# Performance work log

Hardware: AMD Instinct MI355X
Metric: run time of the kernel (lower is better)

The kernel has to match this reference:

```python
import jax, jax.numpy as jnp
import numpy as np

N_USERS = 8192
D = 128
E = 262144        # known edges (nonzero_idx rows)
K = 131072        # static pad size for data-dependent candidate extraction
COS_THR = 0.3
TAU = 0.2


def setup_inputs() -> dict:
    key = jax.random.key(0)
    k1, k2, k3, k4 = jax.random.split(key, 4)
    user_emb = jax.random.normal(k1, (N_USERS, D), dtype=jnp.float32)
    nonzero_idx = jax.random.randint(k2, (E, 2), 0, N_USERS)
    W = jax.random.normal(k3, (2, 2 * D), dtype=jnp.float32) * 0.05  # mlp_s weight [2, 2*latent]
    b = jnp.zeros((2,), dtype=jnp.float32)                            # mlp_s bias
    gumbel_noise = jax.random.gumbel(k4, (E + K, 2), dtype=jnp.float32)
    return {"user_emb": user_emb, "W": W, "b": b,
            "gumbel_noise": gumbel_noise, "nonzero_idx": nonzero_idx}


def reference(user_emb, W, b, gumbel_noise, nonzero_idx):
    n = user_emb.shape[0]
    # ---- get_candidate_pair ----
    norm = jnp.linalg.norm(user_emb, axis=1, keepdims=True)
    u = user_emb / jnp.maximum(norm, 1e-12)          # F.normalize(dim=1)
    cos = u @ u.T                                    # [n, n]
    diag = jnp.arange(n)
    cos = cos.at[diag, diag].set(-1.0)               # fill_diagonal_(-1)
    cos = cos.at[nonzero_idx[:, 0], nonzero_idx[:, 1]].set(-1.0)
    mask = cos > COS_THR
    # static-size nonzero; padded slots point at (0,0) where cos == -1,
    # so they behave as invalid candidates (weight 0 downstream).
    ci, cj = jnp.nonzero(mask, size=K, fill_value=0)
    cand_vals = cos[ci, cj]                          # padded entries = -1
    cand_idx = jnp.stack([ci, cj], axis=1)           # [K, 2]

    # ---- forward ----
    pair_idx = jnp.concatenate([nonzero_idx, cand_idx], axis=0)   # [E+K, 2]
    u_emb = user_emb[pair_idx[:, 0]]
    v_emb = user_emb[pair_idx[:, 1]]
    concat_emb = jnp.concatenate([u_emb, v_emb], axis=1)          # [E+K, 2D]
    logits = concat_emb @ W.T + b                                 # [E+K, 2]

    # hard gumbel-softmax (straight-through)
    y_soft = jax.nn.softmax((logits + gumbel_noise) / TAU, axis=-1)
    y_hard = jax.nn.one_hot(jnp.argmax(y_soft, axis=-1), 2, dtype=y_soft.dtype)
    gumbel_output = y_hard + y_soft - jax.lax.stop_gradient(y_soft)
    gumbel_retain = gumbel_output[:, 0]                           # [E+K]

    # ---- get_edge_weight ----
    cand_w = jnp.maximum(cand_vals, 0.0)                          # masked_fill(<0, 0)
    weights = jnp.concatenate([jnp.ones((E,), dtype=cand_w.dtype), cand_w])
    w = gumbel_retain * weights                                   # [E+K]
    gumbel_01 = w
    gumbel_retain_w = jnp.concatenate([w[:, None], w[:, None]], axis=0)  # [2(E+K), 1]
    return gumbel_01, gumbel_retain_w, pair_idx
```

## Files before the change

### kernel.cpp

```cpp
#include <hip/hip_runtime.h>
#include <hip/hip_bf16.h>
#include <math.h>

#define N_USERS 8192
#define DIMS    128
#define EDGES   262144
#define KCAND   131072
#define NTOT    (EDGES + KCAND)
#define LISTCAP 131072
#define CAPB    2048
#define NTILES  528
#define COS_THR 0.3f
#define EPS_SEL 6e-3f
#define LOGIT_MARGIN 2e-3f
#define DEADKEY 0xFFFFFFFFu

typedef short bf16x8 __attribute__((ext_vector_type(8)));
typedef float f32x4  __attribute__((ext_vector_type(4)));


__global__ __launch_bounds__(256) void prep_k(const float* __restrict__ x,
                                              const float* __restrict__ W,
                                              const int* __restrict__ nz,
                                              float* __restrict__ un,
                                              unsigned short* __restrict__ u0,
                                              float4* __restrict__ P,
                                              unsigned* __restrict__ excl) {
  if (blockIdx.x < 256) {
#pragma clang fp contract(off)
    const int tid  = threadIdx.x;
    const int rloc = tid >> 3;
    const int j    = tid & 7;
    const int i    = blockIdx.x * 32 + rloc;
    const float* r = x + (size_t)i * DIMS;

    float vals[16];
    float a = 0.f;
#pragma unroll
    for (int b8 = 0; b8 < 16; ++b8) {
      float t = r[b8 * 8 + j];
      vals[b8] = t;
      a = a + t * t;
    }
    a = a + __shfl_xor(a, 1, 64);
    a = a + __shfl_xor(a, 2, 64);
    float s = a + __shfl_xor(a, 4, 64);
    float n = (float)sqrt((double)s);
    n = fmaxf(n, 1e-12f);

    unsigned short* slab = u0 + (size_t)(i >> 7) * 16384 + (i & 127) * 8;
    float p0 = 0.f, p1 = 0.f, p2 = 0.f, p3 = 0.f;
#pragma unroll
    for (int b8 = 0; b8 < 16; ++b8) {
      int k = b8 * 8 + j;
      float t = vals[b8];
      float v = t / n;
      un[(size_t)i * DIMS + k] = v;
      __hip_bfloat16 h = __float2bfloat16(v);
      slab[(size_t)b8 * 1024 + j] = *(unsigned short*)&h;
      p0 = fmaf(t, W[k], p0);
      p1 = fmaf(t, W[128 + k], p1);
      p2 = fmaf(t, W[256 + k], p2);
      p3 = fmaf(t, W[384 + k], p3);
    }
#pragma unroll
    for (int m = 1; m < 8; m <<= 1) {
      p0 += __shfl_xor(p0, m, 64);
      p1 += __shfl_xor(p1, m, 64);
      p2 += __shfl_xor(p2, m, 64);
      p3 += __shfl_xor(p3, m, 64);
    }
    if (j == 0) P[i] = make_float4(p0, p1, p2, p3);
  } else {
    int t = (blockIdx.x - 256) * 256 + threadIdx.x;
    if (t < EDGES) {
      uint2 e = ((const uint2*)nz)[t];
      atomicOr(&excl[(size_t)e.x * 256 + (e.y >> 5)], 1u << (e.y & 31));
    }
  }
}

__global__ __launch_bounds__(1024) void mfma_pass(const unsigned short* __restrict__ u0,
                                                  uint2* __restrict__ list,
                                                  int* __restrict__ gcount) {
  __shared__ __align__(16) unsigned short As[2][16][128][8];
  __shared__ __align__(16) unsigned short Bs[2][16][128][8];
  __shared__ uint2 svec[CAPB];
  __shared__ int lcnt, lbase;

  const int tid  = threadIdx.x;
  const int lane = tid & 63;
  const int wv   = tid >> 6;
  const int quad = lane >> 4;
  const int l15  = lane & 15;
  const int wm   = wv >> 2;
  const int wn   = wv & 3;

  int rem = blockIdx.x, cj = 0;
  while (rem >= cj + 1) { rem -= cj + 1; ++cj; }
  const int ri = rem;
  const int I0 = ri * 256, J0 = cj * 256;

  if (tid == 0) lcnt = 0;

  const uint4* __restrict__ Asrc = (const uint4*)(u0 + (size_t)ri * 32768);
  const uint4* __restrict__ Bsrc = (const uint4*)(u0 + (size_t)cj * 32768);
  uint4* Ad = (uint4*)As;
  uint4* Bd = (uint4*)Bs;
  {
    uint4 pA[4], pB[4];
#pragma unroll
    for (int it = 0; it < 4; ++it) {
      pA[it] = Asrc[it * 1024 + tid];
      pB[it] = Bsrc[it * 1024 + tid];
    }
#pragma unroll
    for (int it = 0; it < 4; ++it) {
      Ad[it * 1024 + tid] = pA[it];
      Bd[it * 1024 + tid] = pB[it];
    }
  }
  __syncthreads();

  f32x4 acc[4][4];
#pragma unroll
  for (int mt = 0; mt < 4; ++mt)
#pragma unroll
    for (int nt = 0; nt < 4; ++nt)
#pragma unroll
      for (int g = 0; g < 4; ++g) acc[mt][nt][g] = 0.f;

  const int aslab = wm >> 1, arow0 = (wm & 1) * 64;
  const int bslab = wn >> 1, brow0 = (wn & 1) * 64;

#pragma unroll
  for (int kc = 0; kc < 4; ++kc) {
    const int cq = kc * 4 + quad;
    bf16x8 af[4], bf[4];
#pragma unroll
    for (int mt = 0; mt < 4; ++mt)
      af[mt] = *(const bf16x8*)&As[aslab][cq][arow0 + mt * 16 + l15][0];
#pragma unroll
    for (int nt = 0; nt < 4; ++nt)
      bf[nt] = *(const bf16x8*)&Bs[bslab][cq][brow0 + nt * 16 + l15][0];
#pragma unroll
    for (int mt = 0; mt < 4; ++mt)
#pragma unroll
      for (int nt = 0; nt < 4; ++nt)
        acc[mt][nt] = __builtin_amdgcn_mfma_f32_16x16x32_bf16(
            af[mt], bf[nt], acc[mt][nt], 0, 0, 0);
  }

#pragma unroll
  for (int mt = 0; mt < 4; ++mt)
#pragma unroll
    for (int nt = 0; nt < 4; ++nt)
#pragma unroll
      for (int g = 0; g < 4; ++g) {
        float v = acc[mt][nt][g];
        if (v > COS_THR - EPS_SEL) {
          int i = I0 + wm * 64 + mt * 16 + quad * 4 + g;
          int j = J0 + wn * 64 + nt * 16 + l15;
          if (j > i) {
            int idx = atomicAdd(&lcnt, 2);
            if (idx + 1 < CAPB) {
              svec[idx]     = make_uint2(((unsigned)i << 13) | j,
                                         __float_as_uint(v));
              svec[idx + 1] = make_uint2(((unsigned)j << 13) | i,
                                         __float_as_uint(v));
            }
          }
        }
      }

  __syncthreads();
  int n = min(lcnt, CAPB);
  if (tid == 0) lbase = atomicAdd(gcount, n);
  __syncthreads();
  int base = lbase;
  for (int t = tid; t < n; t += 1024) {
    int o = base + t;
    if (o < LISTCAP) list[o] = svec[t];
  }
}

__global__ __launch_bounds__(256) void resolve_hist_k(const float* __restrict__ un,
                                                      const unsigned* __restrict__ excl,
                                                      uint2* __restrict__ list,
                                                      const int* __restrict__ gcount,
                                                      int* __restrict__ row_cnt) {
  int t = blockIdx.x * 256 + threadIdx.x;
  int n = min(*gcount, LISTCAP);
  if (t >= n) return;
  uint2 e = list[t];
  int i = e.x >> 13, j = e.x & 8191;
  unsigned word = excl[(size_t)i * 256 + (j >> 5)];
  bool alive = !((word >> (j & 31)) & 1u);
  float v = __uint_as_float(e.y);
  if (alive && v <= COS_THR + EPS_SEL) {
    const float* a = un + (size_t)i * DIMS;
    const float* b = un + (size_t)j * DIMS;
    float s = 0.f;
    for (int k = 0; k < DIMS; ++k) s = fmaf(a[k], b[k], s);
    alive = (s > COS_THR);
    if (alive) list[t] = make_uint2(e.x, __float_as_uint(s));
  }
  if (!alive) list[t] = make_uint2(DEADKEY, 0u);
  else        atomicAdd(&row_cnt[i], 1);
}

__global__ __launch_bounds__(256) void scan8k(const int* __restrict__ cnt,
                                              int* __restrict__ off) {
  __shared__ int sm[256];
  int t = threadIdx.x;
  int base = t * 32;
  int s = 0;
  for (int i = 0; i < 32; ++i) s += cnt[base + i];
  sm[t] = s;
  __syncthreads();
  int x = s;
  for (int d = 1; d < 256; d <<= 1) {
    int y = (t >= d) ? sm[t - d] : 0;
    __syncthreads();
    x += y;
    sm[t] = x;
    __syncthreads();
  }
  int run = x - s;
  for (int i = 0; i < 32; ++i) { off[base + i] = run; run += cnt[base + i]; }
  if (t == 255) off[N_USERS] = x;
}

__global__ __launch_bounds__(256) void scatter_k(const uint2* __restrict__ list,
                                                 const int* __restrict__ gcount,
                                                 const int* __restrict__ row_off,
                                                 int* __restrict__ row_pos,
                                                 int* __restrict__ cand_i,
                                                 int* __restrict__ cand_j,
                                                 float* __restrict__ cand_v) {
  int t = blockIdx.x * 256 + threadIdx.x;
  int n = min(*gcount, LISTCAP);
  if (t >= n) return;
  uint2 e = list[t];
  if (e.x == DEADKEY) return;
  int i = e.x >> 13, j = e.x & 8191;
  int pos = row_off[i] + atomicAdd(&row_pos[i], 1);
  if (pos < KCAND) {
    cand_i[pos] = i;
    cand_j[pos] = j;
    cand_v[pos] = __uint_as_float(e.y);
  }
}

__global__ __launch_bounds__(256) void sortrow_k(const int* __restrict__ row_off,
                                                 const int* __restrict__ row_cnt,
                                                 int* __restrict__ cand_j,
                                                 float* __restrict__ cand_v) {
  int r = blockIdx.x * 256 + threadIdx.x;
  if (r >= N_USERS) return;
  int o = row_off[r], c = row_cnt[r];
  if (o + c > KCAND) c = max(0, KCAND - o);
  for (int a = 1; a < c; ++a) {
    int jv = cand_j[o + a];
    float vv = cand_v[o + a];
    int b = a - 1;
    while (b >= 0 && cand_j[o + b] > jv) {
      cand_j[o + b + 1] = cand_j[o + b];
      cand_v[o + b + 1] = cand_v[o + b];
      --b;
    }
    cand_j[o + b + 1] = jv;
    cand_v[o + b + 1] = vv;
  }
}

__global__ __launch_bounds__(256) void finalize_k(const float* __restrict__ ue,
                                                  const float* __restrict__ W,
                                                  const float* __restrict__ b,
                                                  const float* __restrict__ g,
                                                  const int* __restrict__ nz,
                                                  const int* __restrict__ cand_i,
                                                  const int* __restrict__ cand_j,
                                                  const float* __restrict__ cand_v,
                                                  const int* __restrict__ row_off,
                                                  const float4* __restrict__ P,
                                                  float* __restrict__ out) {
  int p = blockIdx.x * 256 + threadIdx.x;
  if (p >= NTOT) return;

  int i, j;
  float wgt;
  if (p < EDGES) {
    i = nz[2 * p];
    j = nz[2 * p + 1];
    wgt = 1.0f;
  } else {
    int q = p - EDGES;
    if (q >= row_off[N_USERS]) {
      out[p] = 0.0f;
      out[NTOT + p] = 0.0f;
      out[2 * NTOT + p] = 0.0f;
      out[3 * NTOT + 2 * p + 0] = 0.0f;
      out[3 * NTOT + 2 * p + 1] = 0.0f;
      return;
    }
    i = cand_i[q];
    j = cand_j[q];
    wgt = fmaxf(cand_v[q], 0.0f);
  }

  float4 Pi = P[i], Pj = P[j];
  float l0 = Pi.x + Pj.y + b[0];
  float l1 = Pi.z + Pj.w + b[1];
  float g0 = g[2 * p], g1 = g[2 * p + 1];
  float s0 = l0 + g0, s1 = l1 + g1;

  if (fabsf(s0 - s1) < LOGIT_MARGIN) {
    const float* ri = ue + (size_t)i * DIMS;
    const float* rj = ue + (size_t)j * DIMS;
    float e0 = 0.f, e1 = 0.f;
    for (int k = 0; k < DIMS; ++k) {
      e0 = fmaf(ri[k], W[k], e0);
      e1 = fmaf(ri[k], W[256 + k], e1);
    }
    for (int k = 0; k < DIMS; ++k) {
      e0 = fmaf(rj[k], W[128 + k], e0);
      e1 = fmaf(rj[k], W[384 + k], e1);
    }
    s0 = (e0 + b[0]) + g0;
    s1 = (e1 + b[1]) + g1;
  }

  float w = (s0 >= s1) ? wgt : 0.0f;

  out[p] = w;
  out[NTOT + p] = w;
  out[2 * NTOT + p] = w;
  out[3 * NTOT + 2 * p + 0] = (float)i;
  out[3 * NTOT + 2 * p + 1] = (float)j;
}

extern "C" void kernel_launch(void* const* d_in, const int* in_sizes, int n_in,
                              void* d_out, int out_size, void* d_ws, size_t ws_size,
                              hipStream_t stream) {
  (void)in_sizes; (void)n_in; (void)out_size; (void)ws_size;

  const float* user_emb = (const float*)d_in[0];
  const float* W        = (const float*)d_in[1];
  const float* b        = (const float*)d_in[2];
  const float* gnoise   = (const float*)d_in[3];
  const int*   nz       = (const int*)d_in[4];
  float* out = (float*)d_out;

  char* ws = (char*)d_ws;
  float*          un      = (float*)(ws + 0);
  unsigned short* u0      = (unsigned short*)(ws + (4u << 20));
  unsigned*       excl    = (unsigned*)(ws + (6u << 20));
  char*           zbase   = ws + (14u << 20);
  int*            gcount  = (int*)(zbase);
  int*            row_cnt = (int*)(zbase + 64);
  int*            row_pos = (int*)(zbase + 64 + 32768);
  int*            row_off = (int*)(ws + (14u << 20) + (96u << 10));
  uint2*          list    = (uint2*)(ws + (15u << 20));
  int*            cand_i  = (int*)(ws + (16u << 20));
  int*            cand_j  = (int*)(ws + (16u << 20) + (512u << 10));
  float*          cand_v  = (float*)(ws + (17u << 20));
  float4*         P       = (float4*)(ws + (17u << 20) + (512u << 10));

  hipMemsetAsync(excl, 0, (8u << 20) + (96u << 10), stream);

  prep_k<<<256 + EDGES / 256, 256, 0, stream>>>(user_emb, W, nz, un, u0, P, excl);
  mfma_pass<<<NTILES, 1024, 0, stream>>>(u0, list, gcount);
  resolve_hist_k<<<LISTCAP / 256, 256, 0, stream>>>(un, excl, list, gcount,
                                                    row_cnt);
  scan8k<<<1, 256, 0, stream>>>(row_cnt, row_off);
  scatter_k<<<LISTCAP / 256, 256, 0, stream>>>(list, gcount, row_off, row_pos,
                                               cand_i, cand_j, cand_v);
  sortrow_k<<<N_USERS / 256, 256, 0, stream>>>(row_off, row_cnt, cand_j, cand_v);
  finalize_k<<<NTOT / 256, 256, 0, stream>>>(user_emb, W, b, gnoise, nz,
                                             cand_i, cand_j, cand_v, row_off,
                                             P, out);
}
```

Measured before the change: 139.2 us.

## Fuse scan, scatter, row sort and finalize into one tail kernel

```diff
diff --git a/kernel.cpp b/kernel.cpp
--- a/kernel.cpp
+++ b/kernel.cpp
@@ -209,106 +209,13 @@
   else        atomicAdd(&row_cnt[i], 1);
 }
 
-__global__ __launch_bounds__(256) void scan8k(const int* __restrict__ cnt,
-                                              int* __restrict__ off) {
-  __shared__ int sm[256];
-  int t = threadIdx.x;
-  int base = t * 32;
-  int s = 0;
-  for (int i = 0; i < 32; ++i) s += cnt[base + i];
-  sm[t] = s;
-  __syncthreads();
-  int x = s;
-  for (int d = 1; d < 256; d <<= 1) {
-    int y = (t >= d) ? sm[t - d] : 0;
-    __syncthreads();
-    x += y;
-    sm[t] = x;
-    __syncthreads();
-  }
-  int run = x - s;
-  for (int i = 0; i < 32; ++i) { off[base + i] = run; run += cnt[base + i]; }
-  if (t == 255) off[N_USERS] = x;
-}
-
-__global__ __launch_bounds__(256) void scatter_k(const uint2* __restrict__ list,
-                                                 const int* __restrict__ gcount,
-                                                 const int* __restrict__ row_off,
-                                                 int* __restrict__ row_pos,
-                                                 int* __restrict__ cand_i,
-                                                 int* __restrict__ cand_j,
-                                                 float* __restrict__ cand_v) {
-  int t = blockIdx.x * 256 + threadIdx.x;
-  int n = min(*gcount, LISTCAP);
-  if (t >= n) return;
-  uint2 e = list[t];
-  if (e.x == DEADKEY) return;
-  int i = e.x >> 13, j = e.x & 8191;
-  int pos = row_off[i] + atomicAdd(&row_pos[i], 1);
-  if (pos < KCAND) {
-    cand_i[pos] = i;
-    cand_j[pos] = j;
-    cand_v[pos] = __uint_as_float(e.y);
-  }
-}
-
-__global__ __launch_bounds__(256) void sortrow_k(const int* __restrict__ row_off,
-                                                 const int* __restrict__ row_cnt,
-                                                 int* __restrict__ cand_j,
-                                                 float* __restrict__ cand_v) {
-  int r = blockIdx.x * 256 + threadIdx.x;
-  if (r >= N_USERS) return;
-  int o = row_off[r], c = row_cnt[r];
-  if (o + c > KCAND) c = max(0, KCAND - o);
-  for (int a = 1; a < c; ++a) {
-    int jv = cand_j[o + a];
-    float vv = cand_v[o + a];
-    int b = a - 1;
-    while (b >= 0 && cand_j[o + b] > jv) {
-      cand_j[o + b + 1] = cand_j[o + b];
-      cand_v[o + b + 1] = cand_v[o + b];
-      --b;
-    }
-    cand_j[o + b + 1] = jv;
-    cand_v[o + b + 1] = vv;
-  }
-}
-
-__global__ __launch_bounds__(256) void finalize_k(const float* __restrict__ ue,
-                                                  const float* __restrict__ W,
-                                                  const float* __restrict__ b,
-                                                  const float* __restrict__ g,
-                                                  const int* __restrict__ nz,
-                                                  const int* __restrict__ cand_i,
-                                                  const int* __restrict__ cand_j,
-                                                  const float* __restrict__ cand_v,
-                                                  const int* __restrict__ row_off,
-                                                  const float4* __restrict__ P,
-                                                  float* __restrict__ out) {
-  int p = blockIdx.x * 256 + threadIdx.x;
-  if (p >= NTOT) return;
-
-  int i, j;
-  float wgt;
-  if (p < EDGES) {
-    i = nz[2 * p];
-    j = nz[2 * p + 1];
-    wgt = 1.0f;
-  } else {
-    int q = p - EDGES;
-    if (q >= row_off[N_USERS]) {
-      out[p] = 0.0f;
-      out[NTOT + p] = 0.0f;
-      out[2 * NTOT + p] = 0.0f;
-      out[3 * NTOT + 2 * p + 0] = 0.0f;
-      out[3 * NTOT + 2 * p + 1] = 0.0f;
-      return;
-    }
-    i = cand_i[q];
-    j = cand_j[q];
-    wgt = fmaxf(cand_v[q], 0.0f);
-  }
-
+__device__ __forceinline__ void emit_out(int p, int i, int j, float wgt,
+                                         const float4* __restrict__ P,
+                                         const float* __restrict__ b,
+                                         const float* __restrict__ g,
+                                         const float* __restrict__ ue,
+                                         const float* __restrict__ W,
+                                         float* __restrict__ out) {
   float4 Pi = P[i], Pj = P[j];
   float l0 = Pi.x + Pj.y + b[0];
   float l1 = Pi.z + Pj.w + b[1];
@@ -332,12 +239,122 @@
   }
 
   float w = (s0 >= s1) ? wgt : 0.0f;
-
   out[p] = w;
   out[NTOT + p] = w;
   out[2 * NTOT + p] = w;
   out[3 * NTOT + 2 * p + 0] = (float)i;
   out[3 * NTOT + 2 * p + 1] = (float)j;
+}
+
+__global__ __launch_bounds__(256) void tail_k(const uint2* __restrict__ list,
+                                              const int* __restrict__ gcount,
+                                              const int* __restrict__ row_cnt,
+                                              int* __restrict__ cand_i,
+                                              int* __restrict__ cand_j,
+                                              float* __restrict__ cand_v,
+                                              const float* __restrict__ ue,
+                                              const float* __restrict__ W,
+                                              const float* __restrict__ b,
+                                              const float* __restrict__ g,
+                                              const int* __restrict__ nz,
+                                              const float4* __restrict__ P,
+                                              float* __restrict__ out) {
+  __shared__ int s_chunk[256];
+  __shared__ int s_off[32];
+  __shared__ int s_pos[32];
+  __shared__ int s_lo, s_M;
+
+  const int tid = threadIdx.x;
+  const int bo  = blockIdx.x;
+
+  int s = 0;
+  {
+    const int rb = tid * 32;
+    for (int k = 0; k < 32; ++k) s += row_cnt[rb + k];
+  }
+  s_chunk[tid] = s;
+  __syncthreads();
+  int x = s;
+  for (int d = 1; d < 256; d <<= 1) {
+    int y = (tid >= d) ? s_chunk[tid - d] : 0;
+    __syncthreads();
+    x += y;
+    s_chunk[tid] = x;
+    __syncthreads();
+  }
+  if (tid == 255) s_M = x;
+  if (tid == bo)  s_lo = x - s;
+  __syncthreads();
+  if (tid == 0) {
+    int run = s_lo;
+    for (int k = 0; k < 32; ++k) {
+      s_off[k] = run;
+      run += row_cnt[bo * 32 + k];
+    }
+  }
+  if (tid < 32) s_pos[tid] = 0;
+  __syncthreads();
+
+  const int n = min(*gcount, LISTCAP);
+  const int M = s_M;
+
+  for (int t = tid; t < n; t += 256) {
+    uint2 e = list[t];
+    if (e.x == DEADKEY) continue;
+    int i = e.x >> 13;
+    if ((i >> 5) == bo) {
+      int lr = i & 31;
+      int pos = s_off[lr] + atomicAdd(&s_pos[lr], 1);
+      if (pos < KCAND) {
+        cand_i[pos] = i;
+        cand_j[pos] = e.x & 8191;
+        cand_v[pos] = __uint_as_float(e.y);
+      }
+    }
+  }
+  __syncthreads();
+
+  if (tid < 32) {
+    int o = s_off[tid], c = s_pos[tid];
+    if (o + c > KCAND) c = max(0, KCAND - o);
+    for (int a = 1; a < c; ++a) {
+      int jv = cand_j[o + a];
+      float vv = cand_v[o + a];
+      int bq = a - 1;
+      while (bq >= 0 && cand_j[o + bq] > jv) {
+        cand_j[o + bq + 1] = cand_j[o + bq];
+        cand_v[o + bq + 1] = cand_v[o + bq];
+        --bq;
+      }
+      cand_j[o + bq + 1] = jv;
+      cand_v[o + bq + 1] = vv;
+    }
+  }
+  __syncthreads();
+
+  {
+    int lo = s_off[0];
+    int hi = min(s_off[31] + s_pos[31], KCAND);
+    for (int q = lo + tid; q < hi; q += 256) {
+      int ci = cand_i[q], cjj = cand_j[q];
+      float wgt = fmaxf(cand_v[q], 0.0f);
+      emit_out(EDGES + q, ci, cjj, wgt, P, b, g, ue, W, out);
+    }
+  }
+
+  for (int p = bo * 1024 + tid; p < bo * 1024 + 1024; p += 256) {
+    uint2 e = ((const uint2*)nz)[p];
+    emit_out(p, (int)e.x, (int)e.y, 1.0f, P, b, g, ue, W, out);
+  }
+
+  for (int q = M + bo * 256 + tid; q < KCAND; q += 256 * 256) {
+    int p = EDGES + q;
+    out[p] = 0.0f;
+    out[NTOT + p] = 0.0f;
+    out[2 * NTOT + p] = 0.0f;
+    out[3 * NTOT + 2 * p + 0] = 0.0f;
+    out[3 * NTOT + 2 * p + 1] = 0.0f;
+  }
 }
 
 extern "C" void kernel_launch(void* const* d_in, const int* in_sizes, int n_in,
@@ -359,8 +376,6 @@
   char*           zbase   = ws + (14u << 20);
   int*            gcount  = (int*)(zbase);
   int*            row_cnt = (int*)(zbase + 64);
-  int*            row_pos = (int*)(zbase + 64 + 32768);
-  int*            row_off = (int*)(ws + (14u << 20) + (96u << 10));
   uint2*          list    = (uint2*)(ws + (15u << 20));
   int*            cand_i  = (int*)(ws + (16u << 20));
   int*            cand_j  = (int*)(ws + (16u << 20) + (512u << 10));
@@ -373,11 +388,6 @@
   mfma_pass<<<NTILES, 1024, 0, stream>>>(u0, list, gcount);
   resolve_hist_k<<<LISTCAP / 256, 256, 0, stream>>>(un, excl, list, gcount,
                                                     row_cnt);
-  scan8k<<<1, 256, 0, stream>>>(row_cnt, row_off);
-  scatter_k<<<LISTCAP / 256, 256, 0, stream>>>(list, gcount, row_off, row_pos,
-                                               cand_i, cand_j, cand_v);
-  sortrow_k<<<N_USERS / 256, 256, 0, stream>>>(row_off, row_cnt, cand_j, cand_v);
-  finalize_k<<<NTOT / 256, 256, 0, stream>>>(user_emb, W, b, gnoise, nz,
-                                             cand_i, cand_j, cand_v, row_off,
-                                             P, out);
-}
+  tail_k<<<256, 256, 0, stream>>>(list, gcount, row_cnt, cand_i, cand_j, cand_v,
+                                  user_emb, W, b, gnoise, nz, P, out);
+}
```

After: 156.5 us. 12.5% more time.
